# Kernel optimization log

Measured on AMD Instinct MI355X. Metric: run time of the kernel, lower is better.

The kernel has to match this reference:

```python
import jax, jax.numpy as jnp
import numpy as np

DIM = 512
NUM_HEADS = 8


def setup_inputs() -> dict:
    key = jax.random.key(0)
    k1, k2, k3, k4, k5 = jax.random.split(key, 5)
    B, N, C = 4, 4096, DIM
    x = jax.random.normal(k1, (B, N, C), dtype=jnp.float32)
    # Conv1d kernel_size=1 weights, squeezed to [out, in]
    qkv_w = jax.random.normal(k2, (3 * C, C), dtype=jnp.float32) * (C ** -0.5)
    qkv_b = jax.random.normal(k3, (3 * C,), dtype=jnp.float32) * 0.02
    out_w = jax.random.normal(k4, (C, C), dtype=jnp.float32) * (C ** -0.5)
    out_b = jax.random.normal(k5, (C,), dtype=jnp.float32) * 0.02
    return {"x": x, "qkv_w": qkv_w, "qkv_b": qkv_b, "out_w": out_w, "out_b": out_b}


def reference(x, qkv_w, qkv_b, out_w, out_b):
    B, N, C = x.shape
    H = NUM_HEADS
    hd = C // H
    scale = hd ** -0.5
    # 1x1 Conv1d == per-position linear: [B,N,C] x [3C,C] -> [B,N,3C]
    qkv = jnp.einsum('bnc,oc->bno', x, qkv_w) + qkv_b
    qkv = qkv.reshape(B, N, 3, H, hd)
    q, k, v = qkv[:, :, 0], qkv[:, :, 1], qkv[:, :, 2]  # each [B,N,H,hd]
    # NOTE: faithful to the original: q @ k.transpose(-2,-1) contracts head_dim
    # giving an [B,N,H,H] score matrix (attention across heads per position).
    scores = jnp.einsum('bnhd,bngd->bnhg', q, k) * scale
    attn = jax.nn.softmax(scores, axis=-1)
    out = jnp.einsum('bnhg,bngd->bnhd', attn, v)  # [B,N,H,hd]
    # Faithful to original: transpose(1,2) then reshape(B,N,C) interleaves axes.
    out = out.transpose(0, 2, 1, 3).reshape(B, N, C)
    out = jnp.einsum('bnc,oc->bno', out, out_w) + out_b
    return out
```

## Files before the change

### kernel.cpp

```cpp
#include <hip/hip_runtime.h>
#include <hip/hip_bf16.h>

#define DIMC 512
#define SEQ 4096
#define M_TOK 16384
#define N_QKV 1536

typedef __bf16 bfv8 __attribute__((ext_vector_type(8)));
typedef float f32v4 __attribute__((ext_vector_type(4)));
typedef unsigned short u16v8 __attribute__((ext_vector_type(8)));

#define VMCNT(n) asm volatile("s_waitcnt vmcnt(" #n ")" ::: "memory")
#define LGKM0()  asm volatile("s_waitcnt lgkmcnt(0)" ::: "memory")

static __device__ __forceinline__ float bf2f(unsigned short u) {
    union { unsigned int i; float f; } x; x.i = ((unsigned int)u) << 16; return x.f;
}
static __device__ __forceinline__ unsigned short f2bf(float f) {
    union { float f; unsigned int i; } x; x.f = f;
    unsigned int r = x.i + 0x7FFFu + ((x.i >> 16) & 1u);
    return (unsigned short)(r >> 16);
}

static __device__ __forceinline__ void gload_lds16(const void* g, void* s) {
    __builtin_amdgcn_global_load_lds(
        (const __attribute__((address_space(1))) unsigned int*)g,
        (__attribute__((address_space(3))) unsigned int*)s, 16, 0, 0);
}

#define NX8  (M_TOK * DIMC / 8)
#define NWQ8 (N_QKV * DIMC / 8)
#define NWO8 (DIMC * DIMC / 8)
__global__ __launch_bounds__(256) void cvt_all(
    const float* __restrict__ x,  const float* __restrict__ wq,
    const float* __restrict__ wo, unsigned short* __restrict__ xb,
    unsigned short* __restrict__ wqb, unsigned short* __restrict__ wob)
{
    int i = blockIdx.x * 256 + threadIdx.x;
    const float* src; unsigned short* dst; int off;
    if (i < NX8)             { src = x;  dst = xb;  off = i; }
    else if (i < NX8 + NWQ8) { src = wq; dst = wqb; off = i - NX8; }
    else                     { src = wo; dst = wob; off = i - NX8 - NWQ8; }
    const float4* p = (const float4*)src + (size_t)off * 2;
    float4 a = p[0], b = p[1];
    u16v8 o;
    o[0] = f2bf(a.x); o[1] = f2bf(a.y); o[2] = f2bf(a.z); o[3] = f2bf(a.w);
    o[4] = f2bf(b.x); o[5] = f2bf(b.y); o[6] = f2bf(b.z); o[7] = f2bf(b.w);
    *(u16v8*)(dst + (size_t)off * 8) = o;
}

template<bool OUT_BF16>
__global__ __launch_bounds__(512) void gemm_nt_r3(
    const unsigned short* __restrict__ A,
    const unsigned short* __restrict__ B,
    const float* __restrict__ bias,
    void* __restrict__ Cout,
    int M, int N, int K)
{
    __shared__ __align__(16) unsigned short As[3][128 * 32];
    __shared__ __align__(16) unsigned short Bs[3][256 * 32];
    const int tid  = threadIdx.x;
    const int lane = tid & 63;
    const int wid  = tid >> 6;
    const int wm   = wid >> 2;
    const int wn   = wid & 3;
    const int m0 = blockIdx.x * 128;
    const int n0 = blockIdx.y * 256;
    const int frow = lane & 15;
    const int fcol = (lane >> 4) * 8;
    const int NT = K >> 5;

    f32v4 acc[4][4] = {};

    const int arow = tid >> 2;
    const int acol = ((tid & 3) * 8) ^ (((arow >> 1) & 3) << 3);
    const unsigned short* aSrc = A + (size_t)(m0 + arow) * K + acol;
    const unsigned short* bSrc[2];
    #pragma unroll
    for (int r = 0; r < 2; ++r) {
        const int brow = r * 128 + (tid >> 2);
        const int bcol = ((tid & 3) * 8) ^ (((brow >> 1) & 3) << 3);
        bSrc[r] = B + (size_t)(n0 + brow) * K + bcol;
    }
    const int aDst = wid * 512;

#define STAGE(kt, slot)                                                        \
    {                                                                          \
        gload_lds16(aSrc + (kt) * 32, &As[slot][aDst]);                        \
        gload_lds16(bSrc[0] + (kt) * 32, &Bs[slot][aDst]);                     \
        gload_lds16(bSrc[1] + (kt) * 32, &Bs[slot][4096 + aDst]);              \
    }

    STAGE(0, 0)
    STAGE(1, 1)
    VMCNT(3);
    __builtin_amdgcn_s_barrier();

    for (int t = 0; t < NT; ++t) {
        const int slot = t % 3;
        bfv8 af[4], bf[4];
        #pragma unroll
        for (int i = 0; i < 4; ++i) {
            const int r = wm * 64 + i * 16 + frow;
            af[i] = *(const bfv8*)(&As[slot][r * 32 + (fcol ^ (((r >> 1) & 3) << 3))]);
        }
        #pragma unroll
        for (int j = 0; j < 4; ++j) {
            const int r = wn * 64 + j * 16 + frow;
            bf[j] = *(const bfv8*)(&Bs[slot][r * 32 + (fcol ^ (((r >> 1) & 3) << 3))]);
        }
        if (t + 2 < NT) {
            const int ws = (t + 2) % 3;
            STAGE(t + 2, ws)
        }
        LGKM0(); __builtin_amdgcn_sched_barrier(0);
        #pragma unroll
        for (int i = 0; i < 4; ++i)
            #pragma unroll
            for (int j = 0; j < 4; ++j)
                acc[i][j] = __builtin_amdgcn_mfma_f32_16x16x32_bf16(
                    af[i], bf[j], acc[i][j], 0, 0, 0);
        if (t + 2 < NT) { VMCNT(3); } else { VMCNT(0); }
        __builtin_amdgcn_s_barrier();
    }
#undef STAGE

    const int erow = (lane >> 4) * 4;
    const int ecol = lane & 15;
    #pragma unroll
    for (int j = 0; j < 4; ++j) {
        const int col = n0 + wn * 64 + j * 16 + ecol;
        const float bv = bias[col];
        #pragma unroll
        for (int i = 0; i < 4; ++i) {
            const int rbase = m0 + wm * 64 + i * 16 + erow;
            #pragma unroll
            for (int r = 0; r < 4; ++r) {
                const float v = acc[i][j][r] + bv;
                if constexpr (OUT_BF16)
                    ((unsigned short*)Cout)[(size_t)(rbase + r) * N + col] = f2bf(v);
                else
                    ((float*)Cout)[(size_t)(rbase + r) * N + col] = v;
            }
        }
    }
}

__global__ __launch_bounds__(256) void attn_mix2(
    const unsigned short* __restrict__ Y1,
    unsigned short* __restrict__ Y2)
{
    const int tid  = threadIdx.x;
    const int tok  = blockIdx.x * 16 + (tid >> 4);
    const int l16  = tid & 15;
    const int h    = l16 >> 1;
    const int half = l16 & 1;
    const unsigned short* qkv = Y1 + (size_t)tok * N_QKV;

    float qf[32];
    #pragma unroll
    for (int c = 0; c < 4; ++c) {
        u16v8 v = *(const u16v8*)(qkv + h * 64 + half * 32 + c * 8);
        #pragma unroll
        for (int j = 0; j < 8; ++j) qf[c * 8 + j] = bf2f(v[j]);
    }
    float sc[8];
    #pragma unroll
    for (int g = 0; g < 8; ++g) {
        const unsigned short* kp = qkv + DIMC + g * 64 + half * 32;
        float a = 0.f;
        #pragma unroll
        for (int c = 0; c < 4; ++c) {
            u16v8 v = *(const u16v8*)(kp + c * 8);
            #pragma unroll
            for (int j = 0; j < 8; ++j) a = fmaf(qf[c * 8 + j], bf2f(v[j]), a);
        }
        a += __shfl_xor(a, 1);
        sc[g] = a * 0.125f;
    }
    float mx = sc[0];
    #pragma unroll
    for (int g = 1; g < 8; ++g) mx = fmaxf(mx, sc[g]);
    float sum = 0.f;
    #pragma unroll
    for (int g = 0; g < 8; ++g) { sc[g] = __expf(sc[g] - mx); sum += sc[g]; }
    const float inv = 1.f / sum;
    #pragma unroll
    for (int g = 0; g < 8; ++g) sc[g] *= inv;

    float o[32] = {};
    #pragma unroll
    for (int g = 0; g < 8; ++g) {
        const unsigned short* vp = qkv + 2 * DIMC + g * 64 + half * 32;
        #pragma unroll
        for (int c = 0; c < 4; ++c) {
            u16v8 v = *(const u16v8*)(vp + c * 8);
            #pragma unroll
            for (int j = 0; j < 8; ++j) o[c * 8 + j] = fmaf(sc[g], bf2f(v[j]), o[c * 8 + j]);
        }
    }
    const int n = tok & (SEQ - 1);
    const int b = tok >> 12;
    const size_t drow = (size_t)b * SEQ + h * 512 + (n >> 3);
    unsigned short* dst = Y2 + drow * DIMC + ((n & 7) << 6) + half * 32;
    #pragma unroll
    for (int c = 0; c < 4; ++c) {
        u16v8 ov;
        #pragma unroll
        for (int j = 0; j < 8; ++j) ov[j] = f2bf(o[c * 8 + j]);
        *(u16v8*)(dst + c * 8) = ov;
    }
}

extern "C" void kernel_launch(void* const* d_in, const int* in_sizes, int n_in,
                              void* d_out, int out_size, void* d_ws, size_t ws_size,
                              hipStream_t stream) {
    const float* x     = (const float*)d_in[0];
    const float* qkv_w = (const float*)d_in[1];
    const float* qkv_b = (const float*)d_in[2];
    const float* out_w = (const float*)d_in[3];
    const float* out_b = (const float*)d_in[4];
    float* out = (float*)d_out;

    unsigned short* Y1 = (unsigned short*)d_ws;
    unsigned short* Xb = Y1 + (size_t)M_TOK * N_QKV;
    unsigned short* Y2 = Xb;
    unsigned short* Wq = Xb + (size_t)M_TOK * DIMC;
    unsigned short* Wo = Wq + (size_t)N_QKV * DIMC;

    cvt_all<<<(NX8 + NWQ8 + NWO8) / 256, 256, 0, stream>>>(x, qkv_w, out_w, Xb, Wq, Wo);

    gemm_nt_r3<true><<<dim3(M_TOK / 128, N_QKV / 256), 512, 0, stream>>>(
        Xb, Wq, qkv_b, Y1, M_TOK, N_QKV, DIMC);

    attn_mix2<<<M_TOK / 16, 256, 0, stream>>>(Y1, Y2);

    gemm_nt_r3<false><<<dim3(M_TOK / 128, DIMC / 256), 512, 0, stream>>>(
        Y2, Wo, out_b, out, M_TOK, DIMC, DIMC);
}
```

Before: 81.15 us.

## Fuse fp32-to-bf16 conversion of x into the QKV GEMM A-tile loads

After: 92.35 us. 1.14x slower.

```diff
diff --git a/kernel.cpp b/kernel.cpp
--- a/kernel.cpp
+++ b/kernel.cpp
@@ -28,19 +28,16 @@
         (__attribute__((address_space(3))) unsigned int*)s, 16, 0, 0);
 }
 
-#define NX8  (M_TOK * DIMC / 8)
 #define NWQ8 (N_QKV * DIMC / 8)
 #define NWO8 (DIMC * DIMC / 8)
-__global__ __launch_bounds__(256) void cvt_all(
-    const float* __restrict__ x,  const float* __restrict__ wq,
-    const float* __restrict__ wo, unsigned short* __restrict__ xb,
+__global__ __launch_bounds__(256) void cvt_w(
+    const float* __restrict__ wq, const float* __restrict__ wo,
     unsigned short* __restrict__ wqb, unsigned short* __restrict__ wob)
 {
     int i = blockIdx.x * 256 + threadIdx.x;
     const float* src; unsigned short* dst; int off;
-    if (i < NX8)             { src = x;  dst = xb;  off = i; }
-    else if (i < NX8 + NWQ8) { src = wq; dst = wqb; off = i - NX8; }
-    else                     { src = wo; dst = wob; off = i - NX8 - NWQ8; }
+    if (i < NWQ8) { src = wq; dst = wqb; off = i; }
+    else          { src = wo; dst = wob; off = i - NWQ8; }
     const float4* p = (const float4*)src + (size_t)off * 2;
     float4 a = p[0], b = p[1];
     u16v8 o;
@@ -49,12 +46,11 @@
     *(u16v8*)(dst + (size_t)off * 8) = o;
 }
 
-template<bool OUT_BF16>
-__global__ __launch_bounds__(512) void gemm_nt_r3(
-    const unsigned short* __restrict__ A,
+__global__ __launch_bounds__(512) void gemm_qkv_f32a(
+    const float* __restrict__ A,
     const unsigned short* __restrict__ B,
     const float* __restrict__ bias,
-    void* __restrict__ Cout,
+    unsigned short* __restrict__ Cout,
     int M, int N, int K)
 {
     __shared__ __align__(16) unsigned short As[3][128 * 32];
@@ -72,6 +68,121 @@
 
     f32v4 acc[4][4] = {};
 
+    const int arow = wid * 16 + (lane & 15);
+    const int ak0  = (lane >> 4) * 8;
+    const float* aSrcF = A + (size_t)(m0 + arow) * K + ak0;
+    const int aWidx = (arow * 32 + ak0) ^ (((arow >> 1) & 3) << 3);
+
+    const unsigned short* bSrc[2];
+    #pragma unroll
+    for (int r = 0; r < 2; ++r) {
+        const int brow = r * 128 + (tid >> 2);
+        const int bcol = ((tid & 3) * 8) ^ (((brow >> 1) & 3) << 3);
+        bSrc[r] = B + (size_t)(n0 + brow) * K + bcol;
+    }
+    const int bDst = wid * 512;
+
+#define STAGE_B(kt, slot)                                                      \
+    {                                                                          \
+        gload_lds16(bSrc[0] + (kt) * 32, &Bs[slot][bDst]);                     \
+        gload_lds16(bSrc[1] + (kt) * 32, &Bs[slot][4096 + bDst]);              \
+    }
+#define A_ISSUE(kt, v0, v1)                                                    \
+    { v0 = *(const float4*)(aSrcF + (kt) * 32); v1 = *(const float4*)(aSrcF + (kt) * 32 + 4); }
+#define A_WRITE(slot, v0, v1)                                                  \
+    {                                                                          \
+        u16v8 cv_;                                                             \
+        cv_[0] = f2bf(v0.x); cv_[1] = f2bf(v0.y); cv_[2] = f2bf(v0.z);         \
+        cv_[3] = f2bf(v0.w); cv_[4] = f2bf(v1.x); cv_[5] = f2bf(v1.y);         \
+        cv_[6] = f2bf(v1.z); cv_[7] = f2bf(v1.w);                              \
+        *(u16v8*)&As[slot][aWidx] = cv_;                                       \
+    }
+
+    float4 a0x, a0y, a1x, a1y, apx, apy;
+    A_ISSUE(0, a0x, a0y)
+    STAGE_B(0, 0)
+    A_ISSUE(1, a1x, a1y)
+    STAGE_B(1, 1)
+    A_WRITE(0, a0x, a0y)
+    A_WRITE(1, a1x, a1y)
+    VMCNT(2);
+    LGKM0();
+    __builtin_amdgcn_s_barrier();
+
+    for (int t = 0; t < NT; ++t) {
+        const int slot = t % 3;
+        if (t + 2 < NT) {
+            A_ISSUE(t + 2, apx, apy)
+            STAGE_B(t + 2, (t + 2) % 3)
+        }
+        bfv8 af[4], bf[4];
+        #pragma unroll
+        for (int i = 0; i < 4; ++i) {
+            const int r = wm * 64 + i * 16 + frow;
+            af[i] = *(const bfv8*)(&As[slot][r * 32 + (fcol ^ (((r >> 1) & 3) << 3))]);
+        }
+        #pragma unroll
+        for (int j = 0; j < 4; ++j) {
+            const int r = wn * 64 + j * 16 + frow;
+            bf[j] = *(const bfv8*)(&Bs[slot][r * 32 + (fcol ^ (((r >> 1) & 3) << 3))]);
+        }
+        LGKM0(); __builtin_amdgcn_sched_barrier(0);
+        #pragma unroll
+        for (int i = 0; i < 4; ++i)
+            #pragma unroll
+            for (int j = 0; j < 4; ++j)
+                acc[i][j] = __builtin_amdgcn_mfma_f32_16x16x32_bf16(
+                    af[i], bf[j], acc[i][j], 0, 0, 0);
+        if (t + 2 < NT) {
+            A_WRITE((t + 2) % 3, apx, apy)
+            VMCNT(2);
+        } else {
+            VMCNT(0);
+        }
+        __builtin_amdgcn_s_barrier();
+    }
+#undef STAGE_B
+#undef A_ISSUE
+#undef A_WRITE
+
+    const int erow = (lane >> 4) * 4;
+    const int ecol = lane & 15;
+    #pragma unroll
+    for (int j = 0; j < 4; ++j) {
+        const int col = n0 + wn * 64 + j * 16 + ecol;
+        const float bv = bias[col];
+        #pragma unroll
+        for (int i = 0; i < 4; ++i) {
+            const int rbase = m0 + wm * 64 + i * 16 + erow;
+            #pragma unroll
+            for (int r = 0; r < 4; ++r)
+                Cout[(size_t)(rbase + r) * N + col] = f2bf(acc[i][j][r] + bv);
+        }
+    }
+}
+
+__global__ __launch_bounds__(512) void gemm_nt_r3(
+    const unsigned short* __restrict__ A,
+    const unsigned short* __restrict__ B,
+    const float* __restrict__ bias,
+    float* __restrict__ Cout,
+    int M, int N, int K)
+{
+    __shared__ __align__(16) unsigned short As[3][128 * 32];
+    __shared__ __align__(16) unsigned short Bs[3][256 * 32];
+    const int tid  = threadIdx.x;
+    const int lane = tid & 63;
+    const int wid  = tid >> 6;
+    const int wm   = wid >> 2;
+    const int wn   = wid & 3;
+    const int m0 = blockIdx.x * 128;
+    const int n0 = blockIdx.y * 256;
+    const int frow = lane & 15;
+    const int fcol = (lane >> 4) * 8;
+    const int NT = K >> 5;
+
+    f32v4 acc[4][4] = {};
+
     const int arow = tid >> 2;
     const int acol = ((tid & 3) * 8) ^ (((arow >> 1) & 3) << 3);
     const unsigned short* aSrc = A + (size_t)(m0 + arow) * K + acol;
@@ -109,10 +220,7 @@
             const int r = wn * 64 + j * 16 + frow;
             bf[j] = *(const bfv8*)(&Bs[slot][r * 32 + (fcol ^ (((r >> 1) & 3) << 3))]);
         }
-        if (t + 2 < NT) {
-            const int ws = (t + 2) % 3;
-            STAGE(t + 2, ws)
-        }
+        if (t + 2 < NT) STAGE(t + 2, (t + 2) % 3)
         LGKM0(); __builtin_amdgcn_sched_barrier(0);
         #pragma unroll
         for (int i = 0; i < 4; ++i)
@@ -135,13 +243,8 @@
         for (int i = 0; i < 4; ++i) {
             const int rbase = m0 + wm * 64 + i * 16 + erow;
             #pragma unroll
-            for (int r = 0; r < 4; ++r) {
-                const float v = acc[i][j][r] + bv;
-                if constexpr (OUT_BF16)
-                    ((unsigned short*)Cout)[(size_t)(rbase + r) * N + col] = f2bf(v);
-                else
-                    ((float*)Cout)[(size_t)(rbase + r) * N + col] = v;
-            }
+            for (int r = 0; r < 4; ++r)
+                Cout[(size_t)(rbase + r) * N + col] = acc[i][j][r] + bv;
         }
     }
 }
@@ -223,18 +326,17 @@
     float* out = (float*)d_out;
 
     unsigned short* Y1 = (unsigned short*)d_ws;
-    unsigned short* Xb = Y1 + (size_t)M_TOK * N_QKV;
-    unsigned short* Y2 = Xb;
-    unsigned short* Wq = Xb + (size_t)M_TOK * DIMC;
+    unsigned short* Y2 = Y1 + (size_t)M_TOK * N_QKV;
+    unsigned short* Wq = Y2 + (size_t)M_TOK * DIMC;
     unsigned short* Wo = Wq + (size_t)N_QKV * DIMC;
 
-    cvt_all<<<(NX8 + NWQ8 + NWO8) / 256, 256, 0, stream>>>(x, qkv_w, out_w, Xb, Wq, Wo);
-
-    gemm_nt_r3<true><<<dim3(M_TOK / 128, N_QKV / 256), 512, 0, stream>>>(
-        Xb, Wq, qkv_b, Y1, M_TOK, N_QKV, DIMC);
+    cvt_w<<<(NWQ8 + NWO8) / 256, 256, 0, stream>>>(qkv_w, out_w, Wq, Wo);
+
+    gemm_qkv_f32a<<<dim3(M_TOK / 128, N_QKV / 256), 512, 0, stream>>>(
+        x, Wq, qkv_b, Y1, M_TOK, N_QKV, DIMC);
 
     attn_mix2<<<M_TOK / 16, 256, 0, stream>>>(Y1, Y2);
 
-    gemm_nt_r3<false><<<dim3(M_TOK / 128, DIMC / 256), 512, 0, stream>>>(
+    gemm_nt_r3<<<dim3(M_TOK / 128, DIMC / 256), 512, 0, stream>>>(
         Y2, Wo, out_b, out, M_TOK, DIMC, DIMC);
 }
```
